# Kernel tuning notes

Hardware: AMD Instinct MI355X
Metric: run time of the kernel (lower is better)

## Reference

```python
import jax, jax.numpy as jnp
import numpy as np

N = 100000      # num_nodes
E = 400000      # num edges
HID = 128       # hidden_channels (== in_channels, memory dim)
OUT = 64        # out_channels (per head)
HEADS = 4
HD = HEADS * OUT  # 256, TransformerConv concat output dim


def _lin(k, fan_in, fan_out):
    return jax.random.normal(k, (fan_in, fan_out), jnp.float32) * 0.02


def setup_inputs() -> dict:
    key = jax.random.key(0)
    ks = jax.random.split(key, 16)
    return {
        "edge_index": jax.random.randint(ks[0], (2, E), 0, N, dtype=jnp.int64),
        "edge_time": jax.random.randint(ks[1], (E, 1), 0, 1000000, dtype=jnp.int64),
        "x": jax.random.normal(ks[2], (N, HID), jnp.float32),
        "memory": jax.random.normal(ks[3], (N, HID), jnp.float32),  # TGN memory table (detached in fwd)
        # TransformerConv params (lin_query / lin_key / lin_value / lin_skip, all with bias)
        "Wq": _lin(ks[4], HID, HD), "bq": jnp.zeros((HD,), jnp.float32),
        "Wk": _lin(ks[5], HID, HD), "bk": jnp.zeros((HD,), jnp.float32),
        "Wv": _lin(ks[6], HID, HD), "bv": jnp.zeros((HD,), jnp.float32),
        "Wskip": _lin(ks[7], HID, HD), "bskip": jnp.zeros((HD,), jnp.float32),
        # rating MLP: Linear(512,128) -> ReLU -> Linear(128,64) -> ReLU -> Linear(64,1)
        "W1": _lin(ks[8], 2 * HD, 128), "b1": jnp.zeros((128,), jnp.float32),
        "W2": _lin(ks[9], 128, 64), "b2": jnp.zeros((64,), jnp.float32),
        "W3": _lin(ks[10], 64, 1), "b3": jnp.zeros((1,), jnp.float32),
    }


def reference(edge_index, edge_time, x, memory,
              Wq, bq, Wk, bk, Wv, bv, Wskip, bskip,
              W1, b1, W2, b2, W3, b3):
    src, dst = edge_index[0], edge_index[1]
    n = x.shape[0]

    # x = memory.detach() + x
    h = memory + x  # [N, HID]

    # TransformerConv (heads=4, concat=True, root_weight=True)
    q = (h @ Wq + bq).reshape(n, HEADS, OUT)
    k = (h @ Wk + bk).reshape(n, HEADS, OUT)
    v = (h @ Wv + bv).reshape(n, HEADS, OUT)

    # per-edge attention scores: messages flow src -> dst, softmax over in-edges of dst
    scores = jnp.sum(q[dst] * k[src], axis=-1) / jnp.sqrt(jnp.float32(OUT))  # [E, H]
    smax = jax.ops.segment_max(scores, dst, num_segments=n)                   # [N, H]
    e = jnp.exp(scores - smax[dst])
    denom = jax.ops.segment_sum(e, dst, num_segments=n)
    alpha = e / (denom[dst] + 1e-16)                                          # [E, H]

    agg = jax.ops.segment_sum(alpha[:, :, None] * v[src], dst, num_segments=n)  # [N, H, OUT]
    out = agg.reshape(n, HD) + (h @ Wskip + bskip)                              # skip connection

    # interaction embeddings + MLP head (dropout inactive at eval)
    inter = jnp.concatenate([out[src], out[dst]], axis=-1)  # [E, 512]
    hdd = jax.nn.relu(inter @ W1 + b1)
    hdd = jax.nn.relu(hdd @ W2 + b2)
    rating = jax.nn.sigmoid(hdd @ W3 + b3) * 4.0 + 1.0
    return rating[:, 0]
```

## Files before the change

kernel.cpp:

```cpp
#include <hip/hip_runtime.h>
#include <math.h>

#define N_NODES 100000
#define N_EDGES 400000
#define HID 128
#define HEADS 4
#define OUT_C 64
#define HD 256
#define SCAN_CHUNK 1024
#define NB_SCAN ((N_NODES + SCAN_CHUNK - 1) / SCAN_CHUNK)
#define SLAB_STRIDE 4356

typedef __attribute__((ext_vector_type(8))) short bf16x8;
typedef __attribute__((ext_vector_type(4))) float f32x4;

__device__ __forceinline__ unsigned short fbf(float f) {
    unsigned u = __float_as_uint(f);
    unsigned r = (u + 0x7fffu + ((u >> 16) & 1u)) >> 16;
    return (unsigned short)r;
}
__device__ __forceinline__ float bf2f(unsigned short u) {
    return __uint_as_float(((unsigned)u) << 16);
}

__device__ __forceinline__ void gl_lds16(const void* g, void* l) {
    __builtin_amdgcn_global_load_lds(
        (const __attribute__((address_space(1))) unsigned int*)g,
        (__attribute__((address_space(3))) unsigned int*)l,
        16, 0, 0);
}

__global__ __launch_bounds__(256) void k_deg(const int* __restrict__ ei,
                                             int* __restrict__ deg) {
    int e = blockIdx.x * 256 + threadIdx.x;
    if (e < N_EDGES) atomicAdd(&deg[ei[N_EDGES + e]], 1);
}

__global__ __launch_bounds__(256) void k_scan1(const int* __restrict__ deg,
                                               int* __restrict__ rp,
                                               int* __restrict__ bsum) {
    __shared__ int ts[256];
    int b = blockIdx.x, t = threadIdx.x;
    int base = b * SCAN_CHUNK + t * 4;
    int vv[4];
    int s = 0;
#pragma unroll
    for (int i = 0; i < 4; ++i) {
        int d = (base + i < N_NODES) ? deg[base + i] : 0;
        vv[i] = s;
        s += d;
    }
    ts[t] = s;
    __syncthreads();
    for (int off = 1; off < 256; off <<= 1) {
        int x = (t >= off) ? ts[t - off] : 0;
        __syncthreads();
        ts[t] += x;
        __syncthreads();
    }
    int ex = ts[t] - s;
#pragma unroll
    for (int i = 0; i < 4; ++i)
        if (base + i < N_NODES) rp[base + i] = ex + vv[i];
    if (t == 255) bsum[b] = ts[255];
}

__global__ __launch_bounds__(256) void k_scan2(int* __restrict__ bsum) {
    __shared__ int ts[256];
    int t = threadIdx.x;
    int v = (t < NB_SCAN) ? bsum[t] : 0;
    ts[t] = v;
    __syncthreads();
    for (int off = 1; off < 256; off <<= 1) {
        int x = (t >= off) ? ts[t - off] : 0;
        __syncthreads();
        ts[t] += x;
        __syncthreads();
    }
    if (t < NB_SCAN) bsum[t] = ts[t] - v;
}

__global__ __launch_bounds__(256) void k_bucket(const int* __restrict__ ei,
                                                const int* __restrict__ rp,
                                                const int* __restrict__ bsum,
                                                int* __restrict__ cursor,
                                                int* __restrict__ csr_src,
                                                int* __restrict__ csr_dst,
                                                int* __restrict__ csr_eid) {
    int e = blockIdx.x * 256 + threadIdx.x;
    if (e >= N_EDGES) return;
    int src = ei[e];
    int d   = ei[N_EDGES + e];
    int idx = atomicAdd(&cursor[d], 1);
    int s   = rp[d] + bsum[d >> 10] + idx;
    csr_src[s] = src;
    csr_dst[s] = d;
    csr_eid[s] = e;
}

__global__ __launch_bounds__(256) void pack_all(
    const float* __restrict__ Wq, const float* __restrict__ Wk,
    const float* __restrict__ Wv, const float* __restrict__ Ws,
    const float* __restrict__ W1, const float* __restrict__ W2,
    unsigned short* __restrict__ Wp, unsigned short* __restrict__ Wcp,
    unsigned short* __restrict__ W2p) {
    int i = blockIdx.x * 256 + threadIdx.x;
    int lane = i & 63;
    int q = lane >> 4, c = lane & 15;
    if (i < 16384) {
        int nt = (i >> 6) & 15, kt = (i >> 10) & 3, z = i >> 12;
        const float* W = (z == 0) ? Wq : (z == 1) ? Wk : (z == 2) ? Wv : Ws;
#pragma unroll
        for (int j = 0; j < 8; ++j)
            Wp[i * 8 + j] = fbf(W[(kt * 32 + q * 8 + j) * HD + nt * 16 + c]);
    } else if (i < 24576) {
        int ii = i - 16384;
        int nt = (ii >> 6) & 15, kt = ii >> 10;
        int n = nt * 16 + c;
#pragma unroll
        for (int j = 0; j < 8; ++j) {
            int k = kt * 32 + q * 8 + j;
            float v = (n < 128) ? W1[k * 128 + n] : W1[(k + 256) * 128 + (n - 128)];
            Wcp[ii * 8 + j] = fbf(v);
        }
    } else if (i < 25600) {
        int ii = i - 24576;
        int nt = (ii >> 6) & 3, kt = ii >> 8;
#pragma unroll
        for (int j = 0; j < 8; ++j)
            W2p[ii * 8 + j] = fbf(W2[(kt * 32 + q * 8 + j) * 64 + nt * 16 + c]);
    }
}

__global__ __launch_bounds__(256) void k_pre(const float* __restrict__ x,
                                             const float* __restrict__ mem,
                                             unsigned short* __restrict__ H) {
    int idx = blockIdx.x * 256 + threadIdx.x;
    if (idx >= N_NODES * HID / 8) return;
    const float4* x4 = (const float4*)x;
    const float4* m4 = (const float4*)mem;
    float4 a0 = x4[(size_t)idx * 2],     a1 = x4[(size_t)idx * 2 + 1];
    float4 b0 = m4[(size_t)idx * 2],     b1 = m4[(size_t)idx * 2 + 1];
    bf16x8 hv;
    hv[0] = (short)fbf(a0.x + b0.x); hv[1] = (short)fbf(a0.y + b0.y);
    hv[2] = (short)fbf(a0.z + b0.z); hv[3] = (short)fbf(a0.w + b0.w);
    hv[4] = (short)fbf(a1.x + b1.x); hv[5] = (short)fbf(a1.y + b1.y);
    hv[6] = (short)fbf(a1.z + b1.z); hv[7] = (short)fbf(a1.w + b1.w);
    *(bf16x8*)&H[(size_t)idx * 8] = hv;
}

__device__ __forceinline__ void mfma_pass(f32x4 acc[4][4], const short* As,
        const unsigned short* __restrict__ Wp, int z, int w, int l, int q, int c) {
#pragma unroll
    for (int mt = 0; mt < 4; ++mt)
#pragma unroll
        for (int nt = 0; nt < 4; ++nt) acc[mt][nt] = (f32x4){0.f, 0.f, 0.f, 0.f};
#pragma unroll
    for (int kt = 0; kt < 4; ++kt) {
        bf16x8 af[4];
#pragma unroll
        for (int mt = 0; mt < 4; ++mt) {
            int row  = mt * 16 + c;
            int slot = (kt * 4 + q) ^ (row & 7);
            af[mt] = *(const bf16x8*)&As[row * 128 + slot * 8];
        }
#pragma unroll
        for (int nt = 0; nt < 4; ++nt) {
            bf16x8 bw8 = *(const bf16x8*)&Wp[(size_t)(((z * 4 + kt) * 16 + w * 4 + nt) * 64 + l) * 8];
#pragma unroll
            for (int mt = 0; mt < 4; ++mt)
                acc[mt][nt] = __builtin_amdgcn_mfma_f32_16x16x32_bf16(af[mt], bw8, acc[mt][nt], 0, 0, 0);
        }
    }
}

__device__ __forceinline__ void slab_store(short* slab, const f32x4 acc[4][4],
        const float bb[4], int q, int c) {
#pragma unroll
    for (int nt = 0; nt < 4; ++nt)
#pragma unroll
        for (int mt = 0; mt < 4; ++mt)
#pragma unroll
            for (int r = 0; r < 4; ++r)
                slab[(mt * 16 + q * 4 + r) * 68 + nt * 16 + c] =
                    (short)fbf(acc[mt][nt][r] + bb[nt]);
}

__device__ __forceinline__ void store_rows(unsigned short* __restrict__ O,
        const short* slab, int m0, int w, int l) {
    const int srow = l >> 3, schk = l & 7;
#pragma unroll
    for (int j = 0; j < 8; ++j) {
        int row = j * 8 + srow;
        int gr  = m0 + row;
        if (gr < N_NODES)
            *(bf16x8*)&O[(size_t)gr * HD + w * 64 + schk * 8] =
                *(const bf16x8*)&slab[row * 68 + schk * 8];
    }
}

__global__ __launch_bounds__(256, 3) void gemm4(
    const unsigned short* __restrict__ H,
    const unsigned short* __restrict__ Wp,
    const float* __restrict__ bq, const float* __restrict__ bk,
    const float* __restrict__ bv, const float* __restrict__ bs,
    unsigned short* __restrict__ Q, unsigned short* __restrict__ KV,
    unsigned short* __restrict__ S)
{
    __shared__ __align__(16) short As[64 * 128];
    __shared__ __align__(16) short Slab[4 * SLAB_STRIDE];

    const int t = threadIdx.x;
    const int w = t >> 6, l = t & 63;
    const int q = l >> 4, c = l & 15;
    const int y  = blockIdx.y;
    const int m0 = blockIdx.x * 64;

#pragma unroll
    for (int i = 0; i < 4; ++i) {
        int rbase = w * 16 + i * 4;
        int r  = rbase + (l >> 4);
        int gr = m0 + r; if (gr >= N_NODES) gr = N_NODES - 1;
        int ks = (l & 15) ^ (r & 7);
        gl_lds16(&H[(size_t)gr * HID + ks * 8], &As[rbase * 128]);
    }

    const int   zA  = (y == 0) ? 0 : 1;
    const int   zB  = (y == 0) ? 3 : 2;
    const float* bA = (y == 0) ? bq : bk;
    const float* bB = (y == 0) ? bs : bv;
    float bbA[4], bbB[4];
#pragma unroll
    for (int nt = 0; nt < 4; ++nt) {
        bbA[nt] = bA[w * 64 + nt * 16 + c];
        bbB[nt] = bB[w * 64 + nt * 16 + c];
    }

    __syncthreads();

    short* slab = &Slab[w * SLAB_STRIDE];
    f32x4 acc[4][4];
    ushort4 kreg[16];
    const int koff = (l & 15) * 4;
    const short* cslab = &Slab[(l >> 4) * SLAB_STRIDE];

    mfma_pass(acc, As, Wp, zA, w, l, q, c);
    slab_store(slab, acc, bbA, q, c);
    if (y == 0) {
        store_rows(Q, slab, m0, w, l);
    } else {
        __syncthreads();
#pragma unroll
        for (int i = 0; i < 16; ++i)
            kreg[i] = *(const ushort4*)&cslab[(w * 16 + i) * 68 + koff];
        __syncthreads();
    }

    mfma_pass(acc, As, Wp, zB, w, l, q, c);
    slab_store(slab, acc, bbB, q, c);
    if (y == 0) {
        store_rows(S, slab, m0, w, l);
    } else {
        __syncthreads();
#pragma unroll
        for (int i = 0; i < 16; ++i) {
            int gr = m0 + w * 16 + i;
            ushort4 vr = *(const ushort4*)&cslab[(w * 16 + i) * 68 + koff];
            if (gr < N_NODES) {
                bf16x8 ov;
                ov[0] = (short)kreg[i].x; ov[1] = (short)kreg[i].y;
                ov[2] = (short)kreg[i].z; ov[3] = (short)kreg[i].w;
                ov[4] = (short)vr.x;      ov[5] = (short)vr.y;
                ov[6] = (short)vr.z;      ov[7] = (short)vr.w;
                *(bf16x8*)&KV[(size_t)gr * 512 + l * 8] = ov;
            }
        }
    }
}

__global__ __launch_bounds__(256) void k_attn(
    const int* __restrict__ rp, const int* __restrict__ bsum,
    const int* __restrict__ deg, const int* __restrict__ csr_src,
    const unsigned short* __restrict__ Q, const unsigned short* __restrict__ KV,
    const unsigned short* __restrict__ S,
    unsigned short* __restrict__ out)
{
    int node = blockIdx.x * 4 + (threadIdx.x >> 6);
    int l = threadIdx.x & 63;
    if (node >= N_NODES) return;
    int start = rp[node] + bsum[node >> 10];
    int cnt   = deg[node];

    float q0, q1, q2, q3;
    {
        ushort4 u = *(const ushort4*)&Q[(size_t)node * HD + l * 4];
        q0 = bf2f(u.x) * 0.125f; q1 = bf2f(u.y) * 0.125f;
        q2 = bf2f(u.z) * 0.125f; q3 = bf2f(u.w) * 0.125f;
    }

    float d = 0.f;
    float a0 = 0.f, a1 = 0.f, a2 = 0.f, a3 = 0.f;

    int i = 0;
    for (; i + 4 <= cnt; i += 4) {
        int s0 = csr_src[start + i];
        int s1 = csr_src[start + i + 1];
        int s2 = csr_src[start + i + 2];
        int s3 = csr_src[start + i + 3];
        bf16x8 k0 = *(const bf16x8*)&KV[(size_t)s0 * 512 + l * 8];
        bf16x8 k1 = *(const bf16x8*)&KV[(size_t)s1 * 512 + l * 8];
        bf16x8 k2 = *(const bf16x8*)&KV[(size_t)s2 * 512 + l * 8];
        bf16x8 k3 = *(const bf16x8*)&KV[(size_t)s3 * 512 + l * 8];
        float sA = q0 * bf2f((unsigned short)k0[0]) + q1 * bf2f((unsigned short)k0[1])
                 + q2 * bf2f((unsigned short)k0[2]) + q3 * bf2f((unsigned short)k0[3]);
        float sB = q0 * bf2f((unsigned short)k1[0]) + q1 * bf2f((unsigned short)k1[1])
                 + q2 * bf2f((unsigned short)k1[2]) + q3 * bf2f((unsigned short)k1[3]);
        float sC = q0 * bf2f((unsigned short)k2[0]) + q1 * bf2f((unsigned short)k2[1])
                 + q2 * bf2f((unsigned short)k2[2]) + q3 * bf2f((unsigned short)k2[3]);
        float sD = q0 * bf2f((unsigned short)k3[0]) + q1 * bf2f((unsigned short)k3[1])
                 + q2 * bf2f((unsigned short)k3[2]) + q3 * bf2f((unsigned short)k3[3]);
        sA += __shfl_xor(sA, 1); sB += __shfl_xor(sB, 1);
        sC += __shfl_xor(sC, 1); sD += __shfl_xor(sD, 1);
        sA += __shfl_xor(sA, 2); sB += __shfl_xor(sB, 2);
        sC += __shfl_xor(sC, 2); sD += __shfl_xor(sD, 2);
        sA += __shfl_xor(sA, 4); sB += __shfl_xor(sB, 4);
        sC += __shfl_xor(sC, 4); sD += __shfl_xor(sD, 4);
        sA += __shfl_xor(sA, 8); sB += __shfl_xor(sB, 8);
        sC += __shfl_xor(sC, 8); sD += __shfl_xor(sD, 8);
        float eA = __expf(sA), eB = __expf(sB), eC = __expf(sC), eD = __expf(sD);
        d += (eA + eB) + (eC + eD);
        a0 += eA * bf2f((unsigned short)k0[4]) + eB * bf2f((unsigned short)k1[4])
            + eC * bf2f((unsigned short)k2[4]) + eD * bf2f((unsigned short)k3[4]);
        a1 += eA * bf2f((unsigned short)k0[5]) + eB * bf2f((unsigned short)k1[5])
            + eC * bf2f((unsigned short)k2[5]) + eD * bf2f((unsigned short)k3[5]);
        a2 += eA * bf2f((unsigned short)k0[6]) + eB * bf2f((unsigned short)k1[6])
            + eC * bf2f((unsigned short)k2[6]) + eD * bf2f((unsigned short)k3[6]);
        a3 += eA * bf2f((unsigned short)k0[7]) + eB * bf2f((unsigned short)k1[7])
            + eC * bf2f((unsigned short)k2[7]) + eD * bf2f((unsigned short)k3[7]);
    }
    if (i + 2 <= cnt) {
        int s0 = csr_src[start + i];
        int s1 = csr_src[start + i + 1];
        bf16x8 k0 = *(const bf16x8*)&KV[(size_t)s0 * 512 + l * 8];
        bf16x8 k1 = *(const bf16x8*)&KV[(size_t)s1 * 512 + l * 8];
        float sA = q0 * bf2f((unsigned short)k0[0]) + q1 * bf2f((unsigned short)k0[1])
                 + q2 * bf2f((unsigned short)k0[2]) + q3 * bf2f((unsigned short)k0[3]);
        float sB = q0 * bf2f((unsigned short)k1[0]) + q1 * bf2f((unsigned short)k1[1])
                 + q2 * bf2f((unsigned short)k1[2]) + q3 * bf2f((unsigned short)k1[3]);
        sA += __shfl_xor(sA, 1); sB += __shfl_xor(sB, 1);
        sA += __shfl_xor(sA, 2); sB += __shfl_xor(sB, 2);
        sA += __shfl_xor(sA, 4); sB += __shfl_xor(sB, 4);
        sA += __shfl_xor(sA, 8); sB += __shfl_xor(sB, 8);
        float eA = __expf(sA), eB = __expf(sB);
        d += eA + eB;
        a0 += eA * bf2f((unsigned short)k0[4]) + eB * bf2f((unsigned short)k1[4]);
        a1 += eA * bf2f((unsigned short)k0[5]) + eB * bf2f((unsigned short)k1[5]);
        a2 += eA * bf2f((unsigned short)k0[6]) + eB * bf2f((unsigned short)k1[6]);
        a3 += eA * bf2f((unsigned short)k0[7]) + eB * bf2f((unsigned short)k1[7]);
        i += 2;
    }
    if (i < cnt) {
        int s0 = csr_src[start + i];
        bf16x8 k0 = *(const bf16x8*)&KV[(size_t)s0 * 512 + l * 8];
        float sA = q0 * bf2f((unsigned short)k0[0]) + q1 * bf2f((unsigned short)k0[1])
                 + q2 * bf2f((unsigned short)k0[2]) + q3 * bf2f((unsigned short)k0[3]);
        sA += __shfl_xor(sA, 1);
        sA += __shfl_xor(sA, 2);
        sA += __shfl_xor(sA, 4);
        sA += __shfl_xor(sA, 8);
        float eA = __expf(sA);
        d += eA;
        a0 += eA * bf2f((unsigned short)k0[4]);
        a1 += eA * bf2f((unsigned short)k0[5]);
        a2 += eA * bf2f((unsigned short)k0[6]);
        a3 += eA * bf2f((unsigned short)k0[7]);
    }

    float inv = 1.f / (d + 1e-16f);
    ushort4 su = *(const ushort4*)&S[(size_t)node * HD + l * 4];
    ushort4 ov = make_ushort4(fbf(bf2f(su.x) + a0 * inv),
                              fbf(bf2f(su.y) + a1 * inv),
                              fbf(bf2f(su.z) + a2 * inv),
                              fbf(bf2f(su.w) + a3 * inv));
    *(ushort4*)&out[(size_t)node * HD + l * 4] = ov;
}

__global__ __launch_bounds__(256, 4) void pd_gemm(
    const unsigned short* __restrict__ outb,
    const unsigned short* __restrict__ Wcp,
    unsigned short* __restrict__ PD)
{
    __shared__ __align__(16) short sh[4 * 64 * 68];
    short* As = sh;

    const int t = threadIdx.x;
    const int w = t >> 6, l = t & 63;
    const int q = l >> 4, c = l & 15;
    const int m0 = blockIdx.x * 64;

#pragma unroll
    for (int i = 0; i < 8; ++i) {
        int rbase = w * 16 + i * 2;
        int r  = rbase + (l >> 5);
        int gr = m0 + r; if (gr >= N_NODES) gr = N_NODES - 1;
        int s  = (l & 31) ^ (r & 7);
        gl_lds16(&outb[(size_t)gr * HD + s * 8], &As[rbase * 256]);
    }

    f32x4 acc[4][4];
#pragma unroll
    for (int mt = 0; mt < 4; ++mt)
#pragma unroll
        for (int nt = 0; nt < 4; ++nt) acc[mt][nt] = (f32x4){0.f, 0.f, 0.f, 0.f};

    __syncthreads();

#pragma unroll
    for (int kt = 0; kt < 8; ++kt) {
        bf16x8 af[4];
#pragma unroll
        for (int mt = 0; mt < 4; ++mt) {
            int row  = mt * 16 + c;
            int slot = (kt * 4 + q) ^ (row & 7);
            af[mt] = *(const bf16x8*)&As[row * 256 + slot * 8];
        }
#pragma unroll
        for (int nt = 0; nt < 4; ++nt) {
            int ntg = w * 4 + nt;
            bf16x8 bv8 = *(const bf16x8*)&Wcp[(size_t)((kt * 16 + ntg) * 64 + l) * 8];
#pragma unroll
            for (int mt = 0; mt < 4; ++mt)
                acc[mt][nt] = __builtin_amdgcn_mfma_f32_16x16x32_bf16(af[mt], bv8, acc[mt][nt], 0, 0, 0);
        }
    }
    __syncthreads();

    short* slab = &sh[w * 64 * 68];
#pragma unroll
    for (int nt = 0; nt < 4; ++nt)
#pragma unroll
        for (int mt = 0; mt < 4; ++mt)
#pragma unroll
            for (int r = 0; r < 4; ++r)
                slab[(mt * 16 + q * 4 + r) * 68 + nt * 16 + c] =
                    (short)fbf(acc[mt][nt][r]);
    const int srow = l >> 3, schk = l & 7;
#pragma unroll
    for (int j = 0; j < 8; ++j) {
        int row = j * 8 + srow;
        int gr = m0 + row;
        if (gr < N_NODES)
            *(bf16x8*)&PD[(size_t)gr * HD + w * 64 + schk * 8] =
                *(const bf16x8*)&slab[row * 68 + schk * 8];
    }
}

__global__ __launch_bounds__(256) void edge_mlp_pd(
    const int* __restrict__ csr_src, const int* __restrict__ csr_dst,
    const int* __restrict__ csr_eid,
    const unsigned short* __restrict__ PD,
    const float* __restrict__ b1,
    const unsigned short* __restrict__ W2p, const float* __restrict__ b2,
    const float* __restrict__ W3, const float* __restrict__ b3,
    float* __restrict__ rating)
{
    __shared__ __align__(16) char lds[64 * 136 * 2];
    short* h1t = (short*)lds;
    float* h2s = (float*)lds;

    const int t = threadIdx.x;
    const int w = t >> 6, l = t & 63;
    const int q = l >> 4, c = l & 15;
    const int e0 = blockIdx.x * 64;

#pragma unroll
    for (int j = 0; j < 4; ++j) {
        int idx = t + j * 256;
        int row = idx >> 4, ch = idx & 15;
        int src = csr_src[e0 + row];
        int dst = csr_dst[e0 + row];
        bf16x8 pv = *(const bf16x8*)&PD[(size_t)src * HD + ch * 8];
        bf16x8 dv = *(const bf16x8*)&PD[(size_t)dst * HD + 128 + ch * 8];
        float4 ba = *(const float4*)&b1[ch * 8];
        float4 bb = *(const float4*)&b1[ch * 8 + 4];
        bf16x8 hv;
        hv[0] = (short)fbf(fmaxf(bf2f((unsigned short)pv[0]) + bf2f((unsigned short)dv[0]) + ba.x, 0.f));
        hv[1] = (short)fbf(fmaxf(bf2f((unsigned short)pv[1]) + bf2f((unsigned short)dv[1]) + ba.y, 0.f));
        hv[2] = (short)fbf(fmaxf(bf2f((unsigned short)pv[2]) + bf2f((unsigned short)dv[2]) + ba.z, 0.f));
        hv[3] = (short)fbf(fmaxf(bf2f((unsigned short)pv[3]) + bf2f((unsigned short)dv[3]) + ba.w, 0.f));
        hv[4] = (short)fbf(fmaxf(bf2f((unsigned short)pv[4]) + bf2f((unsigned short)dv[4]) + bb.x, 0.f));
        hv[5] = (short)fbf(fmaxf(bf2f((unsigned short)pv[5]) + bf2f((unsigned short)dv[5]) + bb.y, 0.f));
        hv[6] = (short)fbf(fmaxf(bf2f((unsigned short)pv[6]) + bf2f((unsigned short)dv[6]) + bb.z, 0.f));
        hv[7] = (short)fbf(fmaxf(bf2f((unsigned short)pv[7]) + bf2f((unsigned short)dv[7]) + bb.w, 0.f));
        *(bf16x8*)&h1t[row * 136 + ch * 8] = hv;
    }
    __syncthreads();

    f32x4 acc2[4];
#pragma unroll
    for (int i = 0; i < 4; ++i) acc2[i] = (f32x4){0.f, 0.f, 0.f, 0.f};
#pragma unroll
    for (int kt = 0; kt < 4; ++kt) {
        bf16x8 av = *(const bf16x8*)&h1t[(w * 16 + c) * 136 + kt * 32 + q * 8];
#pragma unroll
        for (int nt = 0; nt < 4; ++nt) {
            bf16x8 bv = *(const bf16x8*)&W2p[(size_t)((kt * 4 + nt) * 64 + l) * 8];
            acc2[nt] = __builtin_amdgcn_mfma_f32_16x16x32_bf16(av, bv, acc2[nt], 0, 0, 0);
        }
    }
    __syncthreads();

#pragma unroll
    for (int nt = 0; nt < 4; ++nt) {
        float bv = b2[nt * 16 + c];
#pragma unroll
        for (int r = 0; r < 4; ++r)
            h2s[(w * 16 + q * 4 + r) * 65 + nt * 16 + c] = fmaxf(acc2[nt][r] + bv, 0.f);
    }
    __syncthreads();

    if (t < 64) {
        float a = b3[0];
#pragma unroll 8
        for (int kk = 0; kk < 64; ++kk)
            a += h2s[t * 65 + kk] * W3[kk];
        rating[csr_eid[e0 + t]] = 4.f / (1.f + __expf(-a)) + 1.f;
    }
}

extern "C" void kernel_launch(void* const* d_in, const int* in_sizes, int n_in,
                              void* d_out, int out_size, void* d_ws, size_t ws_size,
                              hipStream_t stream) {
    const int*   ei  = (const int*)d_in[0];
    const float* x   = (const float*)d_in[2];
    const float* mem = (const float*)d_in[3];
    const float* Wq  = (const float*)d_in[4];
    const float* bq  = (const float*)d_in[5];
    const float* Wk  = (const float*)d_in[6];
    const float* bk  = (const float*)d_in[7];
    const float* Wv  = (const float*)d_in[8];
    const float* bv  = (const float*)d_in[9];
    const float* Ws  = (const float*)d_in[10];
    const float* bs  = (const float*)d_in[11];
    const float* W1  = (const float*)d_in[12];
    const float* b1  = (const float*)d_in[13];
    const float* W2  = (const float*)d_in[14];
    const float* b2  = (const float*)d_in[15];
    const float* W3  = (const float*)d_in[16];
    const float* b3  = (const float*)d_in[17];
    float* rating = (float*)d_out;

    unsigned short* Q = (unsigned short*)d_ws;
    const size_t NHDe = (size_t)N_NODES * HD;
    unsigned short* KV = Q + NHDe;
    unsigned short* S  = KV + 2 * NHDe;
    unsigned short* H  = S + NHDe;
    int* rp      = (int*)(H + (size_t)N_NODES * HID);
    int* deg     = rp + N_NODES;
    int* cursor  = deg + N_NODES;
    int* csr_src = cursor + N_NODES;
    int* csr_dst = csr_src + N_EDGES;
    int* csr_eid = csr_dst + N_EDGES;
    int* bsum    = csr_eid + N_EDGES;
    unsigned short* Wp  = (unsigned short*)(bsum + 128);
    unsigned short* Wcp = Wp + 16384 * 8;
    unsigned short* W2p = Wcp + 8192 * 8;
    unsigned short* PD  = KV;

    const int eblk  = (N_EDGES + 255) / 256;
    const int wgrid = (N_NODES + 3) / 4;
    const int pblk  = (N_NODES * HID / 8 + 255) / 256;

    hipMemsetAsync(deg, 0, sizeof(int) * 2 * N_NODES, stream);
    k_deg<<<eblk, 256, 0, stream>>>(ei, deg);
    k_scan1<<<NB_SCAN, 256, 0, stream>>>(deg, rp, bsum);
    k_scan2<<<1, 256, 0, stream>>>(bsum);
    k_bucket<<<eblk, 256, 0, stream>>>(ei, rp, bsum, cursor, csr_src, csr_dst, csr_eid);
    pack_all<<<100, 256, 0, stream>>>(Wq, Wk, Wv, Ws, W1, W2, Wp, Wcp, W2p);

    k_pre<<<pblk, 256, 0, stream>>>(x, mem, H);

    gemm4<<<dim3((N_NODES + 63) / 64, 2), dim3(256), 0, stream>>>(
        H, Wp, bq, bk, bv, bs, Q, KV, S);

    k_attn<<<wgrid, 256, 0, stream>>>(rp, bsum, deg, csr_src, Q, KV, S, Q);

    pd_gemm<<<(N_NODES + 63) / 64, 256, 0, stream>>>(Q, Wcp, PD);

    edge_mlp_pd<<<N_EDGES / 64, 256, 0, stream>>>(
        csr_src, csr_dst, csr_eid, PD, b1, W2p, b2, W3, b3, rating);
}
```

Baseline: 422.7 us.

## Fuse attention aggregation into PD GEMM via LDS staging

Merges the per-node attention kernel into the following projection GEMM. Each 512-thread block computes attention outputs for 64 nodes and writes them straight into swizzled LDS, then runs the MFMA GEMM on them. This removes a full global write and read-back of the node output tensor and one kernel launch. PD now aliases Q instead of KV, because KV is still read by other blocks during the fused kernel. The final MLP dot product is also spread across 4 threads per edge with shuffles. The cost is that each wave walks 8 nodes in sequence, which may hide gather latency less well than one node per wave.

```diff
diff --git a/kernel.cpp b/kernel.cpp
--- a/kernel.cpp
+++ b/kernel.cpp
@@ -10,6 +10,7 @@
 #define SCAN_CHUNK 1024
 #define NB_SCAN ((N_NODES + SCAN_CHUNK - 1) / SCAN_CHUNK)
 #define SLAB_STRIDE 4356
+#define PSLAB_W 2576
 
 typedef __attribute__((ext_vector_type(8))) short bf16x8;
 typedef __attribute__((ext_vector_type(4))) float f32x4;
@@ -278,119 +279,15 @@
     }
 }
 
-__global__ __launch_bounds__(256) void k_attn(
+__global__ __launch_bounds__(512, 6) void attn_pd(
     const int* __restrict__ rp, const int* __restrict__ bsum,
     const int* __restrict__ deg, const int* __restrict__ csr_src,
     const unsigned short* __restrict__ Q, const unsigned short* __restrict__ KV,
     const unsigned short* __restrict__ S,
-    unsigned short* __restrict__ out)
-{
-    int node = blockIdx.x * 4 + (threadIdx.x >> 6);
-    int l = threadIdx.x & 63;
-    if (node >= N_NODES) return;
-    int start = rp[node] + bsum[node >> 10];
-    int cnt   = deg[node];
-
-    float q0, q1, q2, q3;
-    {
-        ushort4 u = *(const ushort4*)&Q[(size_t)node * HD + l * 4];
-        q0 = bf2f(u.x) * 0.125f; q1 = bf2f(u.y) * 0.125f;
-        q2 = bf2f(u.z) * 0.125f; q3 = bf2f(u.w) * 0.125f;
-    }
-
-    float d = 0.f;
-    float a0 = 0.f, a1 = 0.f, a2 = 0.f, a3 = 0.f;
-
-    int i = 0;
-    for (; i + 4 <= cnt; i += 4) {
-        int s0 = csr_src[start + i];
-        int s1 = csr_src[start + i + 1];
-        int s2 = csr_src[start + i + 2];
-        int s3 = csr_src[start + i + 3];
-        bf16x8 k0 = *(const bf16x8*)&KV[(size_t)s0 * 512 + l * 8];
-        bf16x8 k1 = *(const bf16x8*)&KV[(size_t)s1 * 512 + l * 8];
-        bf16x8 k2 = *(const bf16x8*)&KV[(size_t)s2 * 512 + l * 8];
-        bf16x8 k3 = *(const bf16x8*)&KV[(size_t)s3 * 512 + l * 8];
-        float sA = q0 * bf2f((unsigned short)k0[0]) + q1 * bf2f((unsigned short)k0[1])
-                 + q2 * bf2f((unsigned short)k0[2]) + q3 * bf2f((unsigned short)k0[3]);
-        float sB = q0 * bf2f((unsigned short)k1[0]) + q1 * bf2f((unsigned short)k1[1])
-                 + q2 * bf2f((unsigned short)k1[2]) + q3 * bf2f((unsigned short)k1[3]);
-        float sC = q0 * bf2f((unsigned short)k2[0]) + q1 * bf2f((unsigned short)k2[1])
-                 + q2 * bf2f((unsigned short)k2[2]) + q3 * bf2f((unsigned short)k2[3]);
-        float sD = q0 * bf2f((unsigned short)k3[0]) + q1 * bf2f((unsigned short)k3[1])
-                 + q2 * bf2f((unsigned short)k3[2]) + q3 * bf2f((unsigned short)k3[3]);
-        sA += __shfl_xor(sA, 1); sB += __shfl_xor(sB, 1);
-        sC += __shfl_xor(sC, 1); sD += __shfl_xor(sD, 1);
-        sA += __shfl_xor(sA, 2); sB += __shfl_xor(sB, 2);
-        sC += __shfl_xor(sC, 2); sD += __shfl_xor(sD, 2);
-        sA += __shfl_xor(sA, 4); sB += __shfl_xor(sB, 4);
-        sC += __shfl_xor(sC, 4); sD += __shfl_xor(sD, 4);
-        sA += __shfl_xor(sA, 8); sB += __shfl_xor(sB, 8);
-        sC += __shfl_xor(sC, 8); sD += __shfl_xor(sD, 8);
-        float eA = __expf(sA), eB = __expf(sB), eC = __expf(sC), eD = __expf(sD);
-        d += (eA + eB) + (eC + eD);
-        a0 += eA * bf2f((unsigned short)k0[4]) + eB * bf2f((unsigned short)k1[4])
-            + eC * bf2f((unsigned short)k2[4]) + eD * bf2f((unsigned short)k3[4]);
-        a1 += eA * bf2f((unsigned short)k0[5]) + eB * bf2f((unsigned short)k1[5])
-            + eC * bf2f((unsigned short)k2[5]) + eD * bf2f((unsigned short)k3[5]);
-        a2 += eA * bf2f((unsigned short)k0[6]) + eB * bf2f((unsigned short)k1[6])
-            + eC * bf2f((unsigned short)k2[6]) + eD * bf2f((unsigned short)k3[6]);
-        a3 += eA * bf2f((unsigned short)k0[7]) + eB * bf2f((unsigned short)k1[7])
-            + eC * bf2f((unsigned short)k2[7]) + eD * bf2f((unsigned short)k3[7]);
-    }
-    if (i + 2 <= cnt) {
-        int s0 = csr_src[start + i];
-        int s1 = csr_src[start + i + 1];
-        bf16x8 k0 = *(const bf16x8*)&KV[(size_t)s0 * 512 + l * 8];
-        bf16x8 k1 = *(const bf16x8*)&KV[(size_t)s1 * 512 + l * 8];
-        float sA = q0 * bf2f((unsigned short)k0[0]) + q1 * bf2f((unsigned short)k0[1])
-                 + q2 * bf2f((unsigned short)k0[2]) + q3 * bf2f((unsigned short)k0[3]);
-        float sB = q0 * bf2f((unsigned short)k1[0]) + q1 * bf2f((unsigned short)k1[1])
-                 + q2 * bf2f((unsigned short)k1[2]) + q3 * bf2f((unsigned short)k1[3]);
-        sA += __shfl_xor(sA, 1); sB += __shfl_xor(sB, 1);
-        sA += __shfl_xor(sA, 2); sB += __shfl_xor(sB, 2);
-        sA += __shfl_xor(sA, 4); sB += __shfl_xor(sB, 4);
-        sA += __shfl_xor(sA, 8); sB += __shfl_xor(sB, 8);
-        float eA = __expf(sA), eB = __expf(sB);
-        d += eA + eB;
-        a0 += eA * bf2f((unsigned short)k0[4]) + eB * bf2f((unsigned short)k1[4]);
-        a1 += eA * bf2f((unsigned short)k0[5]) + eB * bf2f((unsigned short)k1[5]);
-        a2 += eA * bf2f((unsigned short)k0[6]) + eB * bf2f((unsigned short)k1[6]);
-        a3 += eA * bf2f((unsigned short)k0[7]) + eB * bf2f((unsigned short)k1[7]);
-        i += 2;
-    }
-    if (i < cnt) {
-        int s0 = csr_src[start + i];
-        bf16x8 k0 = *(const bf16x8*)&KV[(size_t)s0 * 512 + l * 8];
-        float sA = q0 * bf2f((unsigned short)k0[0]) + q1 * bf2f((unsigned short)k0[1])
-                 + q2 * bf2f((unsigned short)k0[2]) + q3 * bf2f((unsigned short)k0[3]);
-        sA += __shfl_xor(sA, 1);
-        sA += __shfl_xor(sA, 2);
-        sA += __shfl_xor(sA, 4);
-        sA += __shfl_xor(sA, 8);
-        float eA = __expf(sA);
-        d += eA;
-        a0 += eA * bf2f((unsigned short)k0[4]);
-        a1 += eA * bf2f((unsigned short)k0[5]);
-        a2 += eA * bf2f((unsigned short)k0[6]);
-        a3 += eA * bf2f((unsigned short)k0[7]);
-    }
-
-    float inv = 1.f / (d + 1e-16f);
-    ushort4 su = *(const ushort4*)&S[(size_t)node * HD + l * 4];
-    ushort4 ov = make_ushort4(fbf(bf2f(su.x) + a0 * inv),
-                              fbf(bf2f(su.y) + a1 * inv),
-                              fbf(bf2f(su.z) + a2 * inv),
-                              fbf(bf2f(su.w) + a3 * inv));
-    *(ushort4*)&out[(size_t)node * HD + l * 4] = ov;
-}
-
-__global__ __launch_bounds__(256, 4) void pd_gemm(
-    const unsigned short* __restrict__ outb,
     const unsigned short* __restrict__ Wcp,
     unsigned short* __restrict__ PD)
 {
-    __shared__ __align__(16) short sh[4 * 64 * 68];
+    __shared__ __align__(16) short sh[8 * PSLAB_W];
     short* As = sh;
 
     const int t = threadIdx.x;
@@ -398,22 +295,124 @@
     const int q = l >> 4, c = l & 15;
     const int m0 = blockIdx.x * 64;
 
-#pragma unroll
+    int meta = 0;
+    {
+        int nn = m0 + w * 8 + (l & 7);
+        if (nn < N_NODES) {
+            if (l < 8)       meta = rp[nn] + bsum[nn >> 10];
+            else if (l < 16) meta = deg[nn];
+        }
+    }
+
     for (int i = 0; i < 8; ++i) {
-        int rbase = w * 16 + i * 2;
-        int r  = rbase + (l >> 5);
-        int gr = m0 + r; if (gr >= N_NODES) gr = N_NODES - 1;
-        int s  = (l & 31) ^ (r & 7);
-        gl_lds16(&outb[(size_t)gr * HD + s * 8], &As[rbase * 256]);
-    }
-
-    f32x4 acc[4][4];
+        int row  = w * 8 + i;
+        int node = m0 + row;
+        if (node < N_NODES) {
+            int start = __shfl(meta, i);
+            int cnt   = __shfl(meta, 8 + i);
+
+            float q0, q1, q2, q3;
+            ushort4 su;
+            {
+                ushort4 u = *(const ushort4*)&Q[(size_t)node * HD + l * 4];
+                su = *(const ushort4*)&S[(size_t)node * HD + l * 4];
+                q0 = bf2f(u.x) * 0.125f; q1 = bf2f(u.y) * 0.125f;
+                q2 = bf2f(u.z) * 0.125f; q3 = bf2f(u.w) * 0.125f;
+            }
+
+            float d = 0.f;
+            float a0 = 0.f, a1 = 0.f, a2 = 0.f, a3 = 0.f;
+
+            int i2 = 0;
+            for (; i2 + 4 <= cnt; i2 += 4) {
+                int s0 = csr_src[start + i2];
+                int s1 = csr_src[start + i2 + 1];
+                int s2 = csr_src[start + i2 + 2];
+                int s3 = csr_src[start + i2 + 3];
+                bf16x8 k0 = *(const bf16x8*)&KV[(size_t)s0 * 512 + l * 8];
+                bf16x8 k1 = *(const bf16x8*)&KV[(size_t)s1 * 512 + l * 8];
+                bf16x8 k2 = *(const bf16x8*)&KV[(size_t)s2 * 512 + l * 8];
+                bf16x8 k3 = *(const bf16x8*)&KV[(size_t)s3 * 512 + l * 8];
+                float sA = q0 * bf2f((unsigned short)k0[0]) + q1 * bf2f((unsigned short)k0[1])
+                         + q2 * bf2f((unsigned short)k0[2]) + q3 * bf2f((unsigned short)k0[3]);
+                float sB = q0 * bf2f((unsigned short)k1[0]) + q1 * bf2f((unsigned short)k1[1])
+                         + q2 * bf2f((unsigned short)k1[2]) + q3 * bf2f((unsigned short)k1[3]);
+                float sC = q0 * bf2f((unsigned short)k2[0]) + q1 * bf2f((unsigned short)k2[1])
+                         + q2 * bf2f((unsigned short)k2[2]) + q3 * bf2f((unsigned short)k2[3]);
+                float sD = q0 * bf2f((unsigned short)k3[0]) + q1 * bf2f((unsigned short)k3[1])
+                         + q2 * bf2f((unsigned short)k3[2]) + q3 * bf2f((unsigned short)k3[3]);
+                sA += __shfl_xor(sA, 1); sB += __shfl_xor(sB, 1);
+                sC += __shfl_xor(sC, 1); sD += __shfl_xor(sD, 1);
+                sA += __shfl_xor(sA, 2); sB += __shfl_xor(sB, 2);
+                sC += __shfl_xor(sC, 2); sD += __shfl_xor(sD, 2);
+                sA += __shfl_xor(sA, 4); sB += __shfl_xor(sB, 4);
+                sC += __shfl_xor(sC, 4); sD += __shfl_xor(sD, 4);
+                sA += __shfl_xor(sA, 8); sB += __shfl_xor(sB, 8);
+                sC += __shfl_xor(sC, 8); sD += __shfl_xor(sD, 8);
+                float eA = __expf(sA), eB = __expf(sB), eC = __expf(sC), eD = __expf(sD);
+                d += (eA + eB) + (eC + eD);
+                a0 += eA * bf2f((unsigned short)k0[4]) + eB * bf2f((unsigned short)k1[4])
+                    + eC * bf2f((unsigned short)k2[4]) + eD * bf2f((unsigned short)k3[4]);
+                a1 += eA * bf2f((unsigned short)k0[5]) + eB * bf2f((unsigned short)k1[5])
+                    + eC * bf2f((unsigned short)k2[5]) + eD * bf2f((unsigned short)k3[5]);
+                a2 += eA * bf2f((unsigned short)k0[6]) + eB * bf2f((unsigned short)k1[6])
+                    + eC * bf2f((unsigned short)k2[6]) + eD * bf2f((unsigned short)k3[6]);
+                a3 += eA * bf2f((unsigned short)k0[7]) + eB * bf2f((unsigned short)k1[7])
+                    + eC * bf2f((unsigned short)k2[7]) + eD * bf2f((unsigned short)k3[7]);
+            }
+            if (i2 + 2 <= cnt) {
+                int s0 = csr_src[start + i2];
+                int s1 = csr_src[start + i2 + 1];
+                bf16x8 k0 = *(const bf16x8*)&KV[(size_t)s0 * 512 + l * 8];
+                bf16x8 k1 = *(const bf16x8*)&KV[(size_t)s1 * 512 + l * 8];
+                float sA = q0 * bf2f((unsigned short)k0[0]) + q1 * bf2f((unsigned short)k0[1])
+                         + q2 * bf2f((unsigned short)k0[2]) + q3 * bf2f((unsigned short)k0[3]);
+                float sB = q0 * bf2f((unsigned short)k1[0]) + q1 * bf2f((unsigned short)k1[1])
+                         + q2 * bf2f((unsigned short)k1[2]) + q3 * bf2f((unsigned short)k1[3]);
+                sA += __shfl_xor(sA, 1); sB += __shfl_xor(sB, 1);
+                sA += __shfl_xor(sA, 2); sB += __shfl_xor(sB, 2);
+                sA += __shfl_xor(sA, 4); sB += __shfl_xor(sB, 4);
+                sA += __shfl_xor(sA, 8); sB += __shfl_xor(sB, 8);
+                float eA = __expf(sA), eB = __expf(sB);
+                d += eA + eB;
+                a0 += eA * bf2f((unsigned short)k0[4]) + eB * bf2f((unsigned short)k1[4]);
+                a1 += eA * bf2f((unsigned short)k0[5]) + eB * bf2f((unsigned short)k1[5]);
+                a2 += eA * bf2f((unsigned short)k0[6]) + eB * bf2f((unsigned short)k1[6]);
+                a3 += eA * bf2f((unsigned short)k0[7]) + eB * bf2f((unsigned short)k1[7]);
+                i2 += 2;
+            }
+            if (i2 < cnt) {
+                int s0 = csr_src[start + i2];
+                bf16x8 k0 = *(const bf16x8*)&KV[(size_t)s0 * 512 + l * 8];
+                float sA = q0 * bf2f((unsigned short)k0[0]) + q1 * bf2f((unsigned short)k0[1])
+                         + q2 * bf2f((unsigned short)k0[2]) + q3 * bf2f((unsigned short)k0[3]);
+                sA += __shfl_xor(sA, 1);
+                sA += __shfl_xor(sA, 2);
+                sA += __shfl_xor(sA, 4);
+                sA += __shfl_xor(sA, 8);
+                float eA = __expf(sA);
+                d += eA;
+                a0 += eA * bf2f((unsigned short)k0[4]);
+                a1 += eA * bf2f((unsigned short)k0[5]);
+                a2 += eA * bf2f((unsigned short)k0[6]);
+                a3 += eA * bf2f((unsigned short)k0[7]);
+            }
+
+            float inv = 1.f / (d + 1e-16f);
+            ushort4 ov = make_ushort4(fbf(bf2f(su.x) + a0 * inv),
+                                      fbf(bf2f(su.y) + a1 * inv),
+                                      fbf(bf2f(su.z) + a2 * inv),
+                                      fbf(bf2f(su.w) + a3 * inv));
+            *(ushort4*)&As[row * 256 + (((l >> 1) ^ (row & 7)) << 3) + ((l & 1) << 2)] = ov;
+        }
+    }
+    __syncthreads();
+
+    f32x4 acc[4][2];
 #pragma unroll
     for (int mt = 0; mt < 4; ++mt)
 #pragma unroll
-        for (int nt = 0; nt < 4; ++nt) acc[mt][nt] = (f32x4){0.f, 0.f, 0.f, 0.f};
-
-    __syncthreads();
+        for (int nt = 0; nt < 2; ++nt) acc[mt][nt] = (f32x4){0.f, 0.f, 0.f, 0.f};
 
 #pragma unroll
     for (int kt = 0; kt < 8; ++kt) {
@@ -425,8 +424,8 @@
             af[mt] = *(const bf16x8*)&As[row * 256 + slot * 8];
         }
 #pragma unroll
-        for (int nt = 0; nt < 4; ++nt) {
-            int ntg = w * 4 + nt;
+        for (int nt = 0; nt < 2; ++nt) {
+            int ntg = w * 2 + nt;
             bf16x8 bv8 = *(const bf16x8*)&Wcp[(size_t)((kt * 16 + ntg) * 64 + l) * 8];
 #pragma unroll
             for (int mt = 0; mt < 4; ++mt)
@@ -435,23 +434,25 @@
     }
     __syncthreads();
 
-    short* slab = &sh[w * 64 * 68];
-#pragma unroll
-    for (int nt = 0; nt < 4; ++nt)
+    short* slab = &sh[w * PSLAB_W];
+#pragma unroll
+    for (int nt = 0; nt < 2; ++nt)
 #pragma unroll
         for (int mt = 0; mt < 4; ++mt)
 #pragma unroll
             for (int r = 0; r < 4; ++r)
-                slab[(mt * 16 + q * 4 + r) * 68 + nt * 16 + c] =
+                slab[(mt * 16 + q * 4 + r) * 40 + nt * 16 + c] =
                     (short)fbf(acc[mt][nt][r]);
-    const int srow = l >> 3, schk = l & 7;
-#pragma unroll
-    for (int j = 0; j < 8; ++j) {
-        int row = j * 8 + srow;
-        int gr = m0 + row;
+    __syncthreads();
+
+    const int cc = l & 31;
+    const short* sb = &sh[(cc >> 2) * PSLAB_W + (cc & 3) * 8];
+#pragma unroll
+    for (int i = 0; i < 4; ++i) {
+        int row = w * 8 + i * 2 + (l >> 5);
+        int gr  = m0 + row;
         if (gr < N_NODES)
-            *(bf16x8*)&PD[(size_t)gr * HD + w * 64 + schk * 8] =
-                *(const bf16x8*)&slab[row * 68 + schk * 8];
+            *(bf16x8*)&PD[(size_t)gr * HD + cc * 8] = *(const bf16x8*)&sb[row * 40];
     }
 }
 
@@ -519,12 +520,16 @@
     }
     __syncthreads();
 
-    if (t < 64) {
-        float a = b3[0];
-#pragma unroll 8
-        for (int kk = 0; kk < 64; ++kk)
-            a += h2s[t * 65 + kk] * W3[kk];
-        rating[csr_eid[e0 + t]] = 4.f / (1.f + __expf(-a)) + 1.f;
+    {
+        int e = t >> 2, part = t & 3;
+        float a = 0.f;
+#pragma unroll
+        for (int kk = 0; kk < 16; ++kk)
+            a += h2s[e * 65 + part * 16 + kk] * W3[part * 16 + kk];
+        a += __shfl_xor(a, 1);
+        a += __shfl_xor(a, 2);
+        if (part == 0)
+            rating[csr_eid[e0 + e]] = 4.f / (1.f + __expf(-(a + b3[0]))) + 1.f;
     }
 }
 
@@ -565,11 +570,11 @@
     unsigned short* Wp  = (unsigned short*)(bsum + 128);
     unsigned short* Wcp = Wp + 16384 * 8;
     unsigned short* W2p = Wcp + 8192 * 8;
-    unsigned short* PD  = KV;
+    unsigned short* PD  = Q;
 
     const int eblk  = (N_EDGES + 255) / 256;
-    const int wgrid = (N_NODES + 3) / 4;
     const int pblk  = (N_NODES * HID / 8 + 255) / 256;
+    const int gblk  = (N_NODES + 63) / 64;
 
     hipMemsetAsync(deg, 0, sizeof(int) * 2 * N_NODES, stream);
     k_deg<<<eblk, 256, 0, stream>>>(ei, deg);
@@ -580,12 +585,10 @@
 
     k_pre<<<pblk, 256, 0, stream>>>(x, mem, H);
 
-    gemm4<<<dim3((N_NODES + 63) / 64, 2), dim3(256), 0, stream>>>(
+    gemm4<<<dim3(gblk, 2), dim3(256), 0, stream>>>(
         H, Wp, bq, bk, bv, bs, Q, KV, S);
 
-    k_attn<<<wgrid, 256, 0, stream>>>(rp, bsum, deg, csr_src, Q, KV, S, Q);
-
-    pd_gemm<<<(N_NODES + 63) / 64, 256, 0, stream>>>(Q, Wcp, PD);
+    attn_pd<<<gblk, 512, 0, stream>>>(rp, bsum, deg, csr_src, Q, KV, S, Wcp, PD);
 
     edge_mlp_pd<<<N_EDGES / 64, 256, 0, stream>>>(
         csr_src, csr_dst, csr_eid, PD, b1, W2p, b2, W3, b3, rating);
```

After: 416.2 us. About the same (-1.5%).
